# Kernel optimization log

Hardware: AMD Instinct MI355X
Metric: run time of the kernel (lower is better)

The kernel has to match this reference:

```python
import jax, jax.numpy as jnp
import numpy as np

# Static hyperparameters (match init_kwargs)
PAD = 4          # one_side_pad_length
KL = 9           # kernel_size (= 2*PAD + 1 so L_out == output_size with stride 1)
STRIDE = 1
NLC = 8          # num_sparse_LC
OUT = 4096       # output_size


def _repeat_lengths():
    padded = OUT + 2 * PAD                      # 4104
    rough = padded // NLC                       # 513
    lens = []
    total = 0
    for i in range(NLC):
        if i == NLC - 1:
            cover = OUT - total
        else:
            cover = rough - 2 * PAD
        lens.append(cover)
        total += cover
    return lens                                  # [505]*7 + [561]


def setup_inputs() -> dict:
    key = jax.random.key(0)
    k1, k2, k3 = jax.random.split(key, 3)
    x = jax.random.normal(k1, (8, 2, 4, 64, 4096), dtype=jnp.float32)
    # weight: (dim_d, dim_k, out, in, num_sparse_LC, 1, kernel_size)
    weight = jax.random.normal(k2, (2, 4, 64, 64, 8, 1, 9), dtype=jnp.float32) * 0.05
    # conv_bias_param: (dim_d, dim_k, out, num_sparse_LC, 1)
    conv_bias_param = jax.random.normal(k3, (2, 4, 64, 8, 1), dtype=jnp.float32) * 0.02
    return {"x": x, "weight": weight, "conv_bias_param": conv_bias_param}


def reference(x, weight, conv_bias_param):
    # x: (b, d, k, in, L)
    x_pad = jnp.pad(x, ((0, 0), (0, 0), (0, 0), (0, 0), (PAD, PAD)))
    # unfold(-1, KL, 1): x_unf[..., l, f] = x_pad[..., l + f]; shape (b,d,k,in,OUT,KL)
    x_unf = jnp.stack([x_pad[..., f:f + OUT] for f in range(KL)], axis=-1)
    lens = _repeat_lengths()
    outs = []
    start = 0
    for i in range(NLC):  # small fixed loop over segments (avoids repeated-weight materialization)
        ln = lens[i]
        w = weight[:, :, :, :, i, 0, :]                 # (d, k, o, in, kl)
        xs = x_unf[:, :, :, :, start:start + ln, :]     # (b, d, k, in, ln, kl)
        o = jnp.einsum('dkoif,bdkilf->bdkol', w, xs)    # (b, d, k, o, ln)
        o = o + conv_bias_param[None, :, :, :, i, :]    # bias broadcasts over b and l
        outs.append(o)
        start += ln
    return jnp.concatenate(outs, axis=-1)               # (b, d, k, o, OUT)
```

## Files before the change

kernel.cpp:

```cpp
#include <hip/hip_runtime.h>

typedef __attribute__((ext_vector_type(8))) short bf16x8;
typedef __attribute__((ext_vector_type(4))) float f32x4;

#define WT2_BYTES (8ull * 8 * 9 * 8192)

#define AS1C(p) ((const __attribute__((address_space(1))) void*)(p))
#define AS3(p)  ((__attribute__((address_space(3))) void*)(p))

static __device__ __forceinline__ ushort f2bf(float f) {
    union { float f; unsigned u; } v; v.f = f;
    unsigned r = v.u + 0x7FFF + ((v.u >> 16) & 1);
    return (ushort)(r >> 16);
}
static __device__ __forceinline__ unsigned cvtpk(float a, float b) {
    unsigned r;
    asm("v_cvt_pk_bf16_f32 %0, %1, %2" : "=v"(r) : "v"(a), "v"(b));
    return r;
}

__global__ __launch_bounds__(256) void wprep3_kernel(const float* __restrict__ w,
                                                     ushort* __restrict__ wt) {
    __shared__ float raw[4608];
    __shared__ ushort row[72 * 64];
    int bid = blockIdx.x;
    int dk = bid >> 6, o = bid & 63;
    const float* src = w + (size_t)bid * 4608;
    int t = threadIdx.x;
    #pragma unroll
    for (int j = 0; j < 18; ++j) raw[t + 256 * j] = src[t + 256 * j];
    __syncthreads();
    int osw = o & 7;
    #pragma unroll
    for (int p = 0; p < 18; ++p) {
        int idx = t + 256 * p;
        int cf = idx >> 6, i = idx & 63;
        int c = cf / 9, f = cf - c * 9;
        row[cf * 64 + ((i >> 3) ^ osw) * 8 + (i & 7)] = f2bf(raw[i * 72 + c * 9 + f]);
    }
    __syncthreads();
    char* wb = (char*)wt + (size_t)dk * 8 * 9 * 8192 + o * 128;
    #pragma unroll
    for (int q = 0; q < 3; ++q) {
        int idx = q * 256 + t;
        if (idx < 576) {
            int cf = idx >> 3, cc = idx & 7;
            *(uint4*)(wb + (size_t)cf * 8192 + cc * 16) = *(const uint4*)&row[cf * 64 + cc * 8];
        }
    }
}

__global__ __launch_bounds__(256, 4) void conv6_kernel(
    const float* __restrict__ x, const ushort* __restrict__ wt,
    const float* __restrict__ bias, float* __restrict__ out)
{
    __shared__ __align__(16) ushort XL[136 * 64];
    __shared__ __align__(16) ushort WL[2 * 4096];

    int bid = blockIdx.x;
    int bdk = bid / 33, tile = bid - bdk * 33;
    int dk = bdk & 7;
    int c, lt;
    if (tile < 28) { c = tile >> 2; lt = tile & 3; } else { c = 7; lt = tile - 28; }
    int Sc = 505 * c, lb = lt << 7;
    int V = ((c == 7) ? 561 : 505) - lb; if (V > 128) V = 128;
    int R0 = Sc + lb;

    int t = threadIdx.x, lane = t & 63, wv = t >> 6;
    int ln16 = lane & 15, g = lane >> 4;
    int wr = wv >> 1, wc = wv & 1;
    int Lw = wr << 6, Ow = wc << 5;

    const char* wsl = (const char*)wt + (size_t)(dk * 8 + c) * 9 * 8192;
    auto stageW = [&](int f, int buf) {
        __builtin_amdgcn_global_load_lds(AS1C(wsl + (size_t)f * 8192 + t * 16),
                                         AS3((char*)WL + buf * 8192 + t * 16), 16, 0, 0);
        __builtin_amdgcn_global_load_lds(AS1C(wsl + (size_t)f * 8192 + 4096 + t * 16),
                                         AS3((char*)WL + buf * 8192 + 4096 + t * 16), 16, 0, 0);
    };
    stageW(0, 0);

    {
        const float* xb = x + ((size_t)(bdk * 64 + wv * 16)) * 4096;
        bool edge = (R0 < 4) || (R0 > 3964);
        #pragma unroll
        for (int k = 0; k < 3; ++k) {
            int r = k * 64 + lane;
            if (r < 136) {
                int xr = R0 + r - 4;
                float v[16];
                if (!edge) {
                    #pragma unroll
                    for (int j = 0; j < 16; ++j) v[j] = xb[(size_t)j * 4096 + xr];
                } else {
                    bool ok = (xr >= 0) && (xr < 4096);
                    int xc = ok ? xr : 0;
                    #pragma unroll
                    for (int j = 0; j < 16; ++j) v[j] = ok ? xb[(size_t)j * 4096 + xc] : 0.0f;
                }
                uint4 A, B;
                A.x = cvtpk(v[0], v[1]);   A.y = cvtpk(v[2], v[3]);
                A.z = cvtpk(v[4], v[5]);   A.w = cvtpk(v[6], v[7]);
                B.x = cvtpk(v[8], v[9]);   B.y = cvtpk(v[10], v[11]);
                B.z = cvtpk(v[12], v[13]); B.w = cvtpk(v[14], v[15]);
                char* base = (char*)XL + r * 128;
                *(uint4*)(base + (((2 * wv)     ^ (r & 7)) * 16)) = A;
                *(uint4*)(base + (((2 * wv + 1) ^ (r & 7)) * 16)) = B;
            }
        }
    }
    __syncthreads();

    f32x4 acc[4][2];
    #pragma unroll
    for (int a0 = 0; a0 < 4; ++a0)
        #pragma unroll
        for (int a1 = 0; a1 < 2; ++a1) acc[a0][a1] = (f32x4){0.f, 0.f, 0.f, 0.f};

    #pragma unroll 1
    for (int f = 0; f < 9; ++f) {
        int buf = f & 1;
        if (f < 8) stageW(f + 1, buf ^ 1);
        int rbase = Lw + ln16 + f;
        int swz = rbase & 7;
        #pragma unroll
        for (int s = 0; s < 2; ++s) {
            int cof = ((s * 4 + g) ^ swz) * 16;
            int wof = buf * 8192 + ((s * 4 + g) ^ (ln16 & 7)) * 16;
            bf16x8 av[4], bv[2];
            #pragma unroll
            for (int mf = 0; mf < 4; ++mf)
                av[mf] = *(const bf16x8*)((const char*)XL + (rbase + mf * 16) * 128 + cof);
            #pragma unroll
            for (int nf = 0; nf < 2; ++nf)
                bv[nf] = *(const bf16x8*)((const char*)WL + wof + (Ow + nf * 16 + ln16) * 128);
            #pragma unroll
            for (int mf = 0; mf < 4; ++mf)
                #pragma unroll
                for (int nf = 0; nf < 2; ++nf)
                    acc[mf][nf] = __builtin_amdgcn_mfma_f32_16x16x32_bf16(av[mf], bv[nf], acc[mf][nf], 0, 0, 0);
        }
        if (f < 8) __syncthreads();
    }

    float* ob = out + ((size_t)(bdk * 64)) * 4096 + Sc + lb;
    #pragma unroll
    for (int nf = 0; nf < 2; ++nf) {
        int o = Ow + nf * 16 + ln16;
        float bvs = bias[(dk * 64 + o) * 8 + c];
        #pragma unroll
        for (int mf = 0; mf < 4; ++mf) {
            int l = Lw + mf * 16 + g * 4;
            f32x4 vv = acc[mf][nf];
            vv[0] += bvs; vv[1] += bvs; vv[2] += bvs; vv[3] += bvs;
            if (l + 4 <= V) {
                *(f32x4*)(ob + (size_t)o * 4096 + l) = vv;
            } else if (l < V) {
                #pragma unroll
                for (int r = 0; r < 4; ++r)
                    if (l + r < V) ob[(size_t)o * 4096 + l + r] = vv[r];
            }
        }
    }
}

extern "C" void kernel_launch(void* const* d_in, const int* in_sizes, int n_in,
                              void* d_out, int out_size, void* d_ws, size_t ws_size,
                              hipStream_t stream) {
    const float* x    = (const float*)d_in[0];
    const float* wgt  = (const float*)d_in[1];
    const float* bias = (const float*)d_in[2];
    float* out        = (float*)d_out;
    ushort* wt2       = (ushort*)d_ws;

    hipLaunchKernelGGL(wprep3_kernel, dim3(512), dim3(256), 0, stream, wgt, wt2);
    hipLaunchKernelGGL(conv6_kernel, dim3(2112), dim3(256), 0, stream, x, wt2, bias, out);
}
```

Before: 56.13 us.

## Make conv kernel persistent with double-buffered X tiles and register-held weights

The conv kernel becomes a persistent grid of 768 blocks that loop over the 2112 tiles. While the current tile's MFMA taps run, each block prefetches the next tile's x slice into a second LDS buffer. Weights are now read straight from global/L2 into registers with a two-deep rotation, replacing the LDS staging and its per-tap barriers. This aims to hide global-load latency and remove block launch and sync overhead. In exchange it uses more registers and LDS (occupancy hint drops from 4 to 3), and weight reads now go uncoalesced through the cache.

```diff
diff --git a/kernel.cpp b/kernel.cpp
--- a/kernel.cpp
+++ b/kernel.cpp
@@ -4,9 +4,6 @@
 typedef __attribute__((ext_vector_type(4))) float f32x4;
 
 #define WT2_BYTES (8ull * 8 * 9 * 8192)
-
-#define AS1C(p) ((const __attribute__((address_space(1))) void*)(p))
-#define AS3(p)  ((__attribute__((address_space(3))) void*)(p))
 
 static __device__ __forceinline__ ushort f2bf(float f) {
     union { float f; unsigned u; } v; v.f = f;
@@ -50,117 +47,162 @@
     }
 }
 
-__global__ __launch_bounds__(256, 4) void conv6_kernel(
+__global__ __launch_bounds__(256, 3) void conv9_kernel(
     const float* __restrict__ x, const ushort* __restrict__ wt,
     const float* __restrict__ bias, float* __restrict__ out)
 {
-    __shared__ __align__(16) ushort XL[136 * 64];
-    __shared__ __align__(16) ushort WL[2 * 4096];
-
-    int bid = blockIdx.x;
-    int bdk = bid / 33, tile = bid - bdk * 33;
-    int dk = bdk & 7;
-    int c, lt;
-    if (tile < 28) { c = tile >> 2; lt = tile & 3; } else { c = 7; lt = tile - 28; }
-    int Sc = 505 * c, lb = lt << 7;
-    int V = ((c == 7) ? 561 : 505) - lb; if (V > 128) V = 128;
-    int R0 = Sc + lb;
+    __shared__ __align__(16) ushort XL[2][136 * 64];
+
+    const int NT = 2112, GS = 768;
 
     int t = threadIdx.x, lane = t & 63, wv = t >> 6;
     int ln16 = lane & 15, g = lane >> 4;
     int wr = wv >> 1, wc = wv & 1;
     int Lw = wr << 6, Ow = wc << 5;
 
-    const char* wsl = (const char*)wt + (size_t)(dk * 8 + c) * 9 * 8192;
-    auto stageW = [&](int f, int buf) {
-        __builtin_amdgcn_global_load_lds(AS1C(wsl + (size_t)f * 8192 + t * 16),
-                                         AS3((char*)WL + buf * 8192 + t * 16), 16, 0, 0);
-        __builtin_amdgcn_global_load_lds(AS1C(wsl + (size_t)f * 8192 + 4096 + t * 16),
-                                         AS3((char*)WL + buf * 8192 + 4096 + t * 16), 16, 0, 0);
-    };
-    stageW(0, 0);
-
-    {
-        const float* xb = x + ((size_t)(bdk * 64 + wv * 16)) * 4096;
-        bool edge = (R0 < 4) || (R0 > 3964);
-        #pragma unroll
-        for (int k = 0; k < 3; ++k) {
-            int r = k * 64 + lane;
-            if (r < 136) {
-                int xr = R0 + r - 4;
-                float v[16];
-                if (!edge) {
-                    #pragma unroll
-                    for (int j = 0; j < 16; ++j) v[j] = xb[(size_t)j * 4096 + xr];
-                } else {
-                    bool ok = (xr >= 0) && (xr < 4096);
-                    int xc = ok ? xr : 0;
-                    #pragma unroll
-                    for (int j = 0; j < 16; ++j) v[j] = ok ? xb[(size_t)j * 4096 + xc] : 0.0f;
-                }
-                uint4 A, B;
-                A.x = cvtpk(v[0], v[1]);   A.y = cvtpk(v[2], v[3]);
-                A.z = cvtpk(v[4], v[5]);   A.w = cvtpk(v[6], v[7]);
-                B.x = cvtpk(v[8], v[9]);   B.y = cvtpk(v[10], v[11]);
-                B.z = cvtpk(v[12], v[13]); B.w = cvtpk(v[14], v[15]);
-                char* base = (char*)XL + r * 128;
-                *(uint4*)(base + (((2 * wv)     ^ (r & 7)) * 16)) = A;
-                *(uint4*)(base + (((2 * wv + 1) ^ (r & 7)) * 16)) = B;
-            }
-        }
-    }
-    __syncthreads();
+    int wo[2][2];
+    #pragma unroll
+    for (int s = 0; s < 2; ++s)
+        #pragma unroll
+        for (int nf = 0; nf < 2; ++nf)
+            wo[s][nf] = (Ow + nf * 16 + ln16) * 128 + (((s * 4 + g) ^ (ln16 & 7)) * 16);
+
+    auto dec = [&](int tid, int& bdk, int& dk, int& c, int& V, int& R0) {
+        bdk = tid / 33; int tile = tid - bdk * 33;
+        dk = bdk & 7;
+        int lt;
+        if (tile < 28) { c = tile >> 2; lt = tile & 3; } else { c = 7; lt = tile - 28; }
+        int lb = lt << 7;
+        V = ((c == 7) ? 561 : 505) - lb; if (V > 128) V = 128;
+        R0 = 505 * c + lb;
+    };
+
+    auto xload = [&](int bdkX, int R0X, int k, float (&v)[16]) {
+        int r = k * 64 + lane;
+        if (r < 136) {
+            const float* xb = x + ((size_t)(bdkX * 64 + wv * 16)) * 4096;
+            int xr = R0X + r - 4;
+            int xc = xr < 0 ? 0 : (xr > 4095 ? 4095 : xr);
+            #pragma unroll
+            for (int q = 0; q < 16; ++q) v[q] = xb[(size_t)q * 4096 + xc];
+        }
+    };
+    auto xwrite = [&](int R0X, int k, float (&v)[16], ushort* dst) {
+        int r = k * 64 + lane;
+        if (r < 136) {
+            int xr = R0X + r - 4;
+            float m = (xr >= 0 && xr < 4096) ? 1.0f : 0.0f;
+            uint4 A, B;
+            A.x = cvtpk(v[0] * m, v[1] * m);   A.y = cvtpk(v[2] * m, v[3] * m);
+            A.z = cvtpk(v[4] * m, v[5] * m);   A.w = cvtpk(v[6] * m, v[7] * m);
+            B.x = cvtpk(v[8] * m, v[9] * m);   B.y = cvtpk(v[10] * m, v[11] * m);
+            B.z = cvtpk(v[12] * m, v[13] * m); B.w = cvtpk(v[14] * m, v[15] * m);
+            char* base = (char*)dst + r * 128;
+            *(uint4*)(base + (((2 * wv)     ^ (r & 7)) * 16)) = A;
+            *(uint4*)(base + (((2 * wv + 1) ^ (r & 7)) * 16)) = B;
+        }
+    };
 
     f32x4 acc[4][2];
-    #pragma unroll
-    for (int a0 = 0; a0 < 4; ++a0)
-        #pragma unroll
-        for (int a1 = 0; a1 < 2; ++a1) acc[a0][a1] = (f32x4){0.f, 0.f, 0.f, 0.f};
-
-    #pragma unroll 1
-    for (int f = 0; f < 9; ++f) {
-        int buf = f & 1;
-        if (f < 8) stageW(f + 1, buf ^ 1);
+    const char* wbase = nullptr;
+
+    auto loadW = [&](bf16x8 (&d)[2][2], int f) {
+        const char* b = wbase + (size_t)f * 8192;
+        #pragma unroll
+        for (int s = 0; s < 2; ++s)
+            #pragma unroll
+            for (int nf = 0; nf < 2; ++nf)
+                d[s][nf] = *(const bf16x8*)(b + wo[s][nf]);
+    };
+    auto tap = [&](const char* xbuf, int f, bf16x8 (&wf)[2][2]) {
         int rbase = Lw + ln16 + f;
         int swz = rbase & 7;
         #pragma unroll
         for (int s = 0; s < 2; ++s) {
             int cof = ((s * 4 + g) ^ swz) * 16;
-            int wof = buf * 8192 + ((s * 4 + g) ^ (ln16 & 7)) * 16;
-            bf16x8 av[4], bv[2];
+            bf16x8 av[4];
             #pragma unroll
             for (int mf = 0; mf < 4; ++mf)
-                av[mf] = *(const bf16x8*)((const char*)XL + (rbase + mf * 16) * 128 + cof);
-            #pragma unroll
-            for (int nf = 0; nf < 2; ++nf)
-                bv[nf] = *(const bf16x8*)((const char*)WL + wof + (Ow + nf * 16 + ln16) * 128);
+                av[mf] = *(const bf16x8*)(xbuf + (rbase + mf * 16) * 128 + cof);
             #pragma unroll
             for (int mf = 0; mf < 4; ++mf)
                 #pragma unroll
                 for (int nf = 0; nf < 2; ++nf)
-                    acc[mf][nf] = __builtin_amdgcn_mfma_f32_16x16x32_bf16(av[mf], bv[nf], acc[mf][nf], 0, 0, 0);
-        }
-        if (f < 8) __syncthreads();
-    }
-
-    float* ob = out + ((size_t)(bdk * 64)) * 4096 + Sc + lb;
-    #pragma unroll
-    for (int nf = 0; nf < 2; ++nf) {
-        int o = Ow + nf * 16 + ln16;
-        float bvs = bias[(dk * 64 + o) * 8 + c];
-        #pragma unroll
-        for (int mf = 0; mf < 4; ++mf) {
-            int l = Lw + mf * 16 + g * 4;
-            f32x4 vv = acc[mf][nf];
-            vv[0] += bvs; vv[1] += bvs; vv[2] += bvs; vv[3] += bvs;
-            if (l + 4 <= V) {
-                *(f32x4*)(ob + (size_t)o * 4096 + l) = vv;
-            } else if (l < V) {
-                #pragma unroll
-                for (int r = 0; r < 4; ++r)
-                    if (l + r < V) ob[(size_t)o * 4096 + l + r] = vv[r];
+                    acc[mf][nf] = __builtin_amdgcn_mfma_f32_16x16x32_bf16(av[mf], wf[s][nf], acc[mf][nf], 0, 0, 0);
+        }
+    };
+
+    int tid = blockIdx.x;
+    int bdk, dk, c, V, R0;
+    dec(tid, bdk, dk, c, V, R0);
+
+    {
+        float v[16];
+        #pragma unroll
+        for (int k = 0; k < 3; ++k) { xload(bdk, R0, k, v); xwrite(R0, k, v, XL[0]); }
+    }
+    int p = 0;
+
+    while (true) {
+        int nxt = tid + GS;
+        bool hn = nxt < NT;
+        int bdkN = 0, dkN = 0, cN = 0, VN = 0, R0N = 0;
+        if (hn) dec(nxt, bdkN, dkN, cN, VN, R0N);
+
+        wbase = (const char*)wt + (size_t)(dk * 8 + c) * 9 * 8192;
+        const char* xcur = (const char*)XL[p];
+        ushort* xnxt = XL[p ^ 1];
+
+        bf16x8 wA[2][2], wB[2][2];
+        loadW(wA, 0);
+        loadW(wB, 1);
+
+        __syncthreads();
+
+        #pragma unroll
+        for (int a0 = 0; a0 < 4; ++a0)
+            #pragma unroll
+            for (int a1 = 0; a1 < 2; ++a1) acc[a0][a1] = (f32x4){0.f, 0.f, 0.f, 0.f};
+
+        float va[16], vb[16];
+        if (hn) xload(bdkN, R0N, 0, va);
+        tap(xcur, 0, wA); loadW(wA, 2);
+        if (hn) xload(bdkN, R0N, 1, vb);
+        tap(xcur, 1, wB); loadW(wB, 3);
+        if (hn) { xwrite(R0N, 0, va, xnxt); xload(bdkN, R0N, 2, va); }
+        tap(xcur, 2, wA); loadW(wA, 4);
+        if (hn) xwrite(R0N, 1, vb, xnxt);
+        tap(xcur, 3, wB); loadW(wB, 5);
+        if (hn) xwrite(R0N, 2, va, xnxt);
+        tap(xcur, 4, wA); loadW(wA, 6);
+        tap(xcur, 5, wB); loadW(wB, 7);
+        tap(xcur, 6, wA); loadW(wA, 8);
+        tap(xcur, 7, wB);
+        tap(xcur, 8, wA);
+
+        float* ob = out + (size_t)(bdk * 64) * 4096 + R0;
+        #pragma unroll
+        for (int nf = 0; nf < 2; ++nf) {
+            int o = Ow + nf * 16 + ln16;
+            float bvs = bias[(dk * 64 + o) * 8 + c];
+            #pragma unroll
+            for (int mf = 0; mf < 4; ++mf) {
+                int l = Lw + mf * 16 + g * 4;
+                f32x4 vv = acc[mf][nf];
+                vv[0] += bvs; vv[1] += bvs; vv[2] += bvs; vv[3] += bvs;
+                if (l + 4 <= V) {
+                    *(f32x4*)(ob + (size_t)o * 4096 + l) = vv;
+                } else if (l < V) {
+                    #pragma unroll
+                    for (int r = 0; r < 4; ++r)
+                        if (l + r < V) ob[(size_t)o * 4096 + l + r] = vv[r];
+                }
             }
         }
+
+        if (!hn) break;
+        tid = nxt; bdk = bdkN; dk = dkN; c = cN; V = VN; R0 = R0N;
+        p ^= 1;
     }
 }
 
@@ -174,5 +216,5 @@
     ushort* wt2       = (ushort*)d_ws;
 
     hipLaunchKernelGGL(wprep3_kernel, dim3(512), dim3(256), 0, stream, wgt, wt2);
-    hipLaunchKernelGGL(conv6_kernel, dim3(2112), dim3(256), 0, stream, x, wt2, bias, out);
-}
+    hipLaunchKernelGGL(conv9_kernel, dim3(768), dim3(256), 0, stream, x, wt2, bias, out);
+}
```

Measured after the change: 57.46 us. +2.4%, slower.
